# Kernel optimization log

Measured on AMD Instinct MI355X. Metric: run time of the kernel, lower is better.

## Reference

```python
import jax, jax.numpy as jnp
import numpy as np

N = 20000   # genes
E = 200000  # global edges
P = 300     # pathways
EP = 2000   # edges per pathway (global node indices)
D = 3       # in_dim == number of omics (forced by nn.Linear(3,1))


def setup_inputs():
    key = jax.random.key(0)
    ks = jax.random.split(key, 20)
    f = lambda i, shape: jax.random.normal(ks[i], shape, dtype=jnp.float32) * 0.1
    return {
        "x": f(0, (N, D)),
        "edge_index": jax.random.randint(ks[1], (2, E), 0, N),
        "path_edges": jax.random.randint(ks[2], (P, 2, EP), 0, N),
        "W_pool": f(3, (D, D)), "b_pool": f(4, (D,)),
        "W_self": f(5, (D, D)), "W_neigh": f(6, (D, D)), "b_conv": f(7, (D,)),
        "sub_Wl": f(8, (P, D, D)), "sub_bl": f(9, (P, D)), "sub_Wr": f(10, (P, D, D)),
        "pool_Wrel": f(11, (P, D, 1)), "pool_Wroot": f(12, (P, D, 1)), "pool_b": f(13, (P, 1)),
        "gate_W": f(14, (P, D, 1)), "gate_b": f(15, (P, 1)),
        "lin_W": f(16, (D, 1)), "lin_b": f(17, (1,)),
        "mlp_W": f(18, (P, 1)), "mlp_b": f(19, (1,)),
    }


def reference(x, edge_index, path_edges, W_pool, b_pool, W_self, W_neigh, b_conv,
              sub_Wl, sub_bl, sub_Wr, pool_Wrel, pool_Wroot, pool_b,
              gate_W, gate_b, lin_W, lin_b, mlp_W, mlp_b):
    n = x.shape[0]
    # add_self_loops on the global edge_index
    loops = jnp.arange(n)
    src = jnp.concatenate([edge_index[0], loops])
    dst = jnp.concatenate([edge_index[1], loops])

    # global SAGEConv with 'pool' aggregator: max_j relu(W_pool h_j), then self + neigh
    hp = jax.nn.relu(x @ W_pool + b_pool)                       # [N,D]
    agg = jax.ops.segment_max(hp[src], dst, num_segments=n)     # [N,D] (self-loops -> no empty segments)
    h = jnp.tanh(x @ W_self + agg @ W_neigh + b_conv)           # [N,D]

    k = int(np.ceil(0.8 * n))  # SAGPooling ratio=0.8 over all N nodes (full x is passed per pathway)

    def per_path(pe, Wl, bl, Wr, Wrel, Wroot, pb, gW, gb):
        s, d = pe[0], pe[1]
        # SAGEConv (mean aggr) on pathway subgraph edges over full node set
        msum = jax.ops.segment_sum(h[s], d, num_segments=n)
        cnt = jax.ops.segment_sum(jnp.ones(s.shape, h.dtype), d, num_segments=n)
        mean = msum / jnp.maximum(cnt, 1.0)[:, None]
        xc = jax.nn.relu(mean @ Wl + bl + h @ Wr)               # [N,D]
        # SAGPooling score via GraphConv (add aggr): W_rel * sum_j x_j + W_root * x + b
        asum = jax.ops.segment_sum(xc[s], d, num_segments=n)
        score = (asum @ Wrel + xc @ Wroot + pb)[:, 0]           # [N]
        topv, perm = jax.lax.top_k(score, k)
        xk = xc[perm] * jnp.tanh(topv)[:, None]                 # [k,D]
        # GlobalAttention readout: softmax gate over kept nodes
        gate = jax.nn.softmax((xk @ gW + gb)[:, 0])             # [k]
        return jax.nn.relu(gate @ xk)                            # [D]

    readout = jax.vmap(per_path)(path_edges, sub_Wl, sub_bl, sub_Wr,
                                 pool_Wrel, pool_Wroot, pool_b, gate_W, gate_b)  # [P,D]
    r = jax.nn.relu(readout @ lin_W + lin_b).T                  # [1,P]
    # mlp: Dropout (identity in eval) -> ReLU -> Linear(P,1) -> Sigmoid
    return jax.nn.sigmoid(jax.nn.relu(r) @ mlp_W + mlp_b)       # [1,1]
```

## Files before the change

kernel.cpp:

```cpp
#include <hip/hip_runtime.h>
#include <math.h>

#define MAXM 2048
#define BMW  640
#define BS   1024
#define NB   2048

__device__ __forceinline__ unsigned fkey(float f){
  unsigned u = __float_as_uint(f);
  return (u & 0x80000000u) ? ~u : (u | 0x80000000u);
}
__device__ __forceinline__ int lbin(float sc, float lo, float scl){
  int b = (int)((sc - lo) * scl);
  return b < 0 ? 0 : (b > NB-1 ? NB-1 : b);
}
__device__ __forceinline__ float fast_tanh(float x){
  float e = __expf(2.f*x);
  return 1.f - 2.f*__builtin_amdgcn_rcpf(e + 1.f);
}
__device__ __forceinline__ void hp_eval(const float* __restrict__ x, int i,
                                        const float* __restrict__ Wp,
                                        const float* __restrict__ bp, float* o){
  float x0 = x[i*3+0], x1 = x[i*3+1], x2 = x[i*3+2];
  #pragma unroll
  for (int j = 0; j < 3; ++j)
    o[j] = fmaxf(x0*Wp[0*3+j] + x1*Wp[1*3+j] + x2*Wp[2*3+j] + bp[j], 0.f);
}

__global__ void k_edge(const float* __restrict__ x, const int* __restrict__ ei,
                       const float* __restrict__ Wp, const float* __restrict__ bp,
                       float* __restrict__ agg, float* __restrict__ acc,
                       unsigned* __restrict__ counter, int E){
  if (blockIdx.x == 0 && threadIdx.x == 0){ acc[0] = 0.f; counter[0] = 0u; }
  int e = blockIdx.x*blockDim.x + threadIdx.x;
  if (e >= E) return;
  int s = ei[e], d = ei[E+e];
  float o[3]; hp_eval(x, s, Wp, bp, o);
  #pragma unroll
  for (int j = 0; j < 3; ++j)
    if (o[j] > 0.f && o[j] > agg[d*4+j])
      atomicMax((int*)&agg[d*4+j], __float_as_int(o[j]));
}

__global__ void k_h2(const float* __restrict__ x, float* __restrict__ hb,
                     const float* __restrict__ Wp, const float* __restrict__ bp,
                     const float* __restrict__ Ws, const float* __restrict__ Wn,
                     const float* __restrict__ bc, int N){
  int i = blockIdx.x*blockDim.x + threadIdx.x;
  if (i >= N) return;
  float hp[3]; hp_eval(x, i, Wp, bp, hp);
  float x0 = x[i*3+0], x1 = x[i*3+1], x2 = x[i*3+2];
  float a0 = fmaxf(hb[i*4+0], hp[0]);
  float a1 = fmaxf(hb[i*4+1], hp[1]);
  float a2 = fmaxf(hb[i*4+2], hp[2]);
  float o[3];
  #pragma unroll
  for (int j = 0; j < 3; ++j){
    float v = x0*Ws[0*3+j] + x1*Ws[1*3+j] + x2*Ws[2*3+j]
            + a0*Wn[0*3+j] + a1*Wn[1*3+j] + a2*Wn[2*3+j] + bc[j];
    o[j] = tanhf(v);
  }
  float4 hv; hv.x = o[0]; hv.y = o[1]; hv.z = o[2]; hv.w = 0.f;
  *reinterpret_cast<float4*>(&hb[i*4]) = hv;
}

__global__ void __launch_bounds__(BS)
k_mega(const float* __restrict__ h, const int* __restrict__ pe,
       const float* __restrict__ sWl, const float* __restrict__ sbl, const float* __restrict__ sWr,
       const float* __restrict__ pWrel, const float* __restrict__ pWroot, const float* __restrict__ pB,
       const float* __restrict__ gW, const float* __restrict__ gB,
       const float* __restrict__ linW, const float* __restrict__ linb,
       const float* __restrict__ mlpW, const float* __restrict__ mlpb,
       float* __restrict__ spG, float* __restrict__ acc, unsigned* __restrict__ counter,
       unsigned* __restrict__ out, int N, int EP, int K, int P){
  __shared__ unsigned bm[BMW];
  __shared__ int      wpfx[BMW];
  __shared__ float    msum[MAXM*4];
  __shared__ unsigned scrA[NB];
  __shared__ unsigned scrB[NB];
  __shared__ unsigned candIdx[NB];
  __shared__ float    wredf[(BS/64)*2];
  __shared__ float    wredA[(BS/64)*4];
  __shared__ float    wredB[(BS/64)*4];
  __shared__ float    s_mn, s_mx;
  __shared__ float    rlo[3], rsc[3];
  __shared__ int      rb[3];
  __shared__ int      s_r, s_C, s_cc, s_done, s_fused;
  __shared__ unsigned s_uT;

  const int p = blockIdx.x;
  const int tid = threadIdx.x;

  float Wl[9], Wr[9], bl[3], wrel[3], wroot[3], gw[3];
  #pragma unroll
  for (int j = 0; j < 9; ++j){ Wl[j] = sWl[p*9+j]; Wr[j] = sWr[p*9+j]; }
  #pragma unroll
  for (int j = 0; j < 3; ++j){
    bl[j] = sbl[p*3+j]; wrel[j] = pWrel[p*3+j];
    wroot[j] = pWroot[p*3+j]; gw[j] = gW[p*3+j];
  }
  float pbv = pB[p], gbv = gB[p];
  float* sp = spG + (size_t)p*N;

  int*   cnt  = (int*)scrA;
  float* adot = (float*)scrB;

  for (int s = tid; s < MAXM; s += BS){
    cnt[s] = 0; adot[s] = 0.f;
    float4 z; z.x = 0.f; z.y = 0.f; z.z = 0.f; z.w = 0.f;
    *reinterpret_cast<float4*>(&msum[s*4]) = z;
  }
  for (int s = tid; s < BMW; s += BS) bm[s] = 0u;
  if (tid == 0){ s_done = 0; s_fused = 0; s_uT = 0u; }
  __syncthreads();

  const int* ps = pe + (size_t)p*2*EP;
  const int* pd = ps + EP;

  for (int e = tid; e < EP; e += BS) atomicOr(&bm[pd[e]>>5], 1u << (pd[e]&31));
  __syncthreads();
  if (tid < 64){
    int l = tid, base = l*10;
    int c[10], s = 0;
    #pragma unroll
    for (int q = 0; q < 10; ++q){ c[q] = __popc(bm[base+q]); s += c[q]; }
    int pre = s;
    #pragma unroll
    for (int off = 1; off < 64; off <<= 1){
      int t = __shfl_up(pre, off);
      if (l >= off) pre += t;
    }
    pre -= s;
    #pragma unroll
    for (int q = 0; q < 10; ++q){ wpfx[base+q] = pre; pre += c[q]; }
  }
  __syncthreads();
  for (int e = tid; e < EP; e += BS){
    int s = ps[e], d = pd[e];
    int r = wpfx[d>>5] + __popc(bm[d>>5] & ((1u << (d&31)) - 1u));
    float4 hs = *reinterpret_cast<const float4*>(&h[s*4]);
    atomicAdd(&cnt[r], 1);
    atomicAdd(&msum[r*4+0], hs.x);
    atomicAdd(&msum[r*4+1], hs.y);
    atomicAdd(&msum[r*4+2], hs.z);
  }
  __syncthreads();
  for (int r = tid; r < MAXM; r += BS){
    int c = cnt[r];
    cnt[r] = 0;
    if (c > 0){
      float inv = 1.f / (float)c;
      msum[r*4+0] *= inv; msum[r*4+1] *= inv; msum[r*4+2] *= inv;
    }
  }
  __syncthreads();
  for (int e = tid; e < EP; e += BS){
    int s = ps[e], d = pd[e];
    float m0=0.f,m1=0.f,m2=0.f;
    unsigned w = bm[s>>5];
    if ((w >> (s&31)) & 1u){
      int rs = wpfx[s>>5] + __popc(w & ((1u << (s&31)) - 1u));
      float4 mv = *reinterpret_cast<const float4*>(&msum[rs*4]);
      m0 = mv.x; m1 = mv.y; m2 = mv.z;
    }
    float4 hv = *reinterpret_cast<const float4*>(&h[s*4]);
    float h0 = hv.x, h1 = hv.y, h2 = hv.z;
    float x0 = fmaxf(m0*Wl[0]+m1*Wl[3]+m2*Wl[6] + bl[0] + h0*Wr[0]+h1*Wr[3]+h2*Wr[6], 0.f);
    float x1 = fmaxf(m0*Wl[1]+m1*Wl[4]+m2*Wl[7] + bl[1] + h0*Wr[1]+h1*Wr[4]+h2*Wr[7], 0.f);
    float x2 = fmaxf(m0*Wl[2]+m1*Wl[5]+m2*Wl[8] + bl[2] + h0*Wr[2]+h1*Wr[5]+h2*Wr[8], 0.f);
    int rd = wpfx[d>>5] + __popc(bm[d>>5] & ((1u << (d&31)) - 1u));
    atomicAdd(&adot[rd], x0*wrel[0] + x1*wrel[1] + x2*wrel[2]);
  }
  __syncthreads();

  float mn = 3.0e38f, mx = -3.0e38f;
  float tl = 0.f, ta0 = 0.f, ta1 = 0.f, ta2 = 0.f;
  for (int i = tid; i < N; i += BS){
    float m0=0.f,m1=0.f,m2=0.f,ad=0.f;
    unsigned w = bm[i>>5];
    if ((w >> (i&31)) & 1u){
      int r = wpfx[i>>5] + __popc(w & ((1u << (i&31)) - 1u));
      float4 mv = *reinterpret_cast<const float4*>(&msum[r*4]);
      m0 = mv.x; m1 = mv.y; m2 = mv.z;
      ad = adot[r];
    }
    float4 hv = *reinterpret_cast<const float4*>(&h[i*4]);
    float h0 = hv.x, h1 = hv.y, h2 = hv.z;
    float x0 = fmaxf(m0*Wl[0]+m1*Wl[3]+m2*Wl[6] + bl[0] + h0*Wr[0]+h1*Wr[3]+h2*Wr[6], 0.f);
    float x1 = fmaxf(m0*Wl[1]+m1*Wl[4]+m2*Wl[7] + bl[1] + h0*Wr[1]+h1*Wr[4]+h2*Wr[7], 0.f);
    float x2 = fmaxf(m0*Wl[2]+m1*Wl[5]+m2*Wl[8] + bl[2] + h0*Wr[2]+h1*Wr[5]+h2*Wr[8], 0.f);
    float sc = ad + x0*wroot[0]+x1*wroot[1]+x2*wroot[2] + pbv;
    sp[i] = sc;
    mn = fminf(mn, sc); mx = fmaxf(mx, sc);
    float tt = fast_tanh(sc);
    float g = fminf(fmaxf(tt*(x0*gw[0]+x1*gw[1]+x2*gw[2]) + gbv, -60.f), 60.f);
    float e = __expf(g);
    float et = e * tt;
    tl += e; ta0 += et*x0; ta1 += et*x1; ta2 += et*x2;
  }
  #pragma unroll
  for (int off = 32; off > 0; off >>= 1){
    mn  = fminf(mn, __shfl_down(mn, off));
    mx  = fmaxf(mx, __shfl_down(mx, off));
    tl  += __shfl_down(tl,  off); ta0 += __shfl_down(ta0, off);
    ta1 += __shfl_down(ta1, off); ta2 += __shfl_down(ta2, off);
  }
  if ((tid & 63) == 0){
    int w = tid >> 6;
    wredf[w*2+0] = mn; wredf[w*2+1] = mx;
    wredA[w*4+0]=tl; wredA[w*4+1]=ta0; wredA[w*4+2]=ta1; wredA[w*4+3]=ta2;
  }
  __syncthreads();
  if (tid == 0){
    float a = 3.0e38f, b = -3.0e38f;
    for (int w = 0; w < BS/64; ++w){ a = fminf(a, wredf[w*2+0]); b = fmaxf(b, wredf[w*2+1]); }
    s_mn = a; s_mx = b; s_r = K;
    if (!(b > a)){ s_uT = fkey(a); s_done = 1; s_fused = 1; }
  }
  __syncthreads();

  unsigned* hist = scrA;
  unsigned* cand = scrB;

  float dl = 0.f, d0 = 0.f, d1 = 0.f, d2 = 0.f;

  for (int t = 0; t < 3; ++t){
    __syncthreads();
    if (s_done) break;
    float lo, hi;
    if (t == 0){ lo = s_mn; hi = s_mx; }
    else { lo = rlo[t-1] + rb[t-1]/rsc[t-1]; hi = rlo[t-1] + (rb[t-1]+1)/rsc[t-1]; }
    float scl = 2047.0f / (hi - lo);
    if (!(hi > lo) || !(scl < 1e37f)){
      if (tid == 0){ s_uT = fkey(lo); s_done = 1; }
      __syncthreads();
      continue;
    }
    if (t > 0){
      for (int b = tid; b < NB; b += BS) hist[b] = 0u;
      __syncthreads();
    }
    if (t == 0){
      if ((N & 3) == 0){
        int G = N >> 2;
        for (int g = tid; g < G; g += BS){
          float4 v = ((const float4*)sp)[g];
          atomicAdd(&hist[lbin(v.x, lo, scl)], 1u);
          atomicAdd(&hist[lbin(v.y, lo, scl)], 1u);
          atomicAdd(&hist[lbin(v.z, lo, scl)], 1u);
          atomicAdd(&hist[lbin(v.w, lo, scl)], 1u);
        }
      } else {
        for (int i = tid; i < N; i += BS) atomicAdd(&hist[lbin(sp[i], lo, scl)], 1u);
      }
    } else {
      for (int i = tid; i < N; i += BS){
        float sc = sp[i];
        bool act = true;
        for (int q = 0; q < t; ++q) act = act && (lbin(sc, rlo[q], rsc[q]) == rb[q]);
        if (act) atomicAdd(&hist[lbin(sc, lo, scl)], 1u);
      }
    }
    __syncthreads();
    if (tid < 64){
      int l = tid;
      unsigned s = 0;
      for (int q = 0; q < 32; ++q) s += hist[l*32+q];
      unsigned S = s;
      #pragma unroll
      for (int off = 1; off < 64; off <<= 1){
        unsigned u2 = __shfl_down(S, off);
        if (l + off < 64) S += u2;
      }
      unsigned suf = S - s;
      unsigned r = (unsigned)s_r;
      int b = -1; unsigned sufnext = 0, cb = 0;
      for (int q = 31; q >= 0; --q){
        unsigned c = hist[l*32+q];
        unsigned nsuf = suf + c;
        if (nsuf >= r && suf < r){ b = l*32+q; sufnext = suf; cb = c; }
        suf = nsuf;
      }
      if (b >= 0){
        rb[t] = b; rlo[t] = lo; rsc[t] = scl;
        s_r = (int)(r - sufnext);
        s_C = (int)cb;
      }
    }
    __syncthreads();
    int C = s_C;
    if (C <= NB){
      if (tid < 1024) hist[tid] = 0u;
      if (tid == 0) s_cc = 0;
      __syncthreads();
      if (t == 0 && (N & 3) == 0){
        const int b0 = rb[0];
        const float l0 = rlo[0], s0 = rsc[0];
        int G = N >> 2;
        for (int g = tid; g < G; g += BS){
          float4 v = ((const float4*)sp)[g];
          #pragma unroll
          for (int u = 0; u < 4; ++u){
            float sc = (u==0)?v.x:((u==1)?v.y:((u==2)?v.z:v.w));
            int b = lbin(sc, l0, s0);
            if (b == b0){
              int ix = atomicAdd(&s_cc, 1);
              if (ix < NB){ cand[ix] = fkey(sc); candIdx[ix] = (unsigned)(g*4+u); }
            } else if (b < b0){
              int i = g*4+u;
              float m0=0.f,m1=0.f,m2=0.f;
              unsigned w = bm[i>>5];
              if ((w >> (i&31)) & 1u){
                int r = wpfx[i>>5] + __popc(w & ((1u << (i&31)) - 1u));
                float4 mv = *reinterpret_cast<const float4*>(&msum[r*4]);
                m0 = mv.x; m1 = mv.y; m2 = mv.z;
              }
              float4 hv = *reinterpret_cast<const float4*>(&h[i*4]);
              float h0 = hv.x, h1 = hv.y, h2 = hv.z;
              float x0 = fmaxf(m0*Wl[0]+m1*Wl[3]+m2*Wl[6] + bl[0] + h0*Wr[0]+h1*Wr[3]+h2*Wr[6], 0.f);
              float x1 = fmaxf(m0*Wl[1]+m1*Wl[4]+m2*Wl[7] + bl[1] + h0*Wr[1]+h1*Wr[4]+h2*Wr[7], 0.f);
              float x2 = fmaxf(m0*Wl[2]+m1*Wl[5]+m2*Wl[8] + bl[2] + h0*Wr[2]+h1*Wr[5]+h2*Wr[8], 0.f);
              float tt = fast_tanh(sc);
              float gg = fminf(fmaxf(tt*(x0*gw[0]+x1*gw[1]+x2*gw[2]) + gbv, -60.f), 60.f);
              float e = __expf(gg);
              float et = e * tt;
              dl += e; d0 += et*x0; d1 += et*x1; d2 += et*x2;
            }
          }
        }
      } else {
        for (int i = tid; i < N; i += BS){
          float sc = sp[i];
          bool iscand = true, isdrop = false;
          for (int q = 0; q <= t; ++q){
            int b = lbin(sc, rlo[q], rsc[q]);
            if (b != rb[q]){ iscand = false; isdrop = (b < rb[q]); break; }
          }
          if (iscand){
            int ix = atomicAdd(&s_cc, 1);
            if (ix < NB){ cand[ix] = fkey(sc); candIdx[ix] = (unsigned)i; }
          } else if (isdrop){
            float m0=0.f,m1=0.f,m2=0.f;
            unsigned w = bm[i>>5];
            if ((w >> (i&31)) & 1u){
              int r = wpfx[i>>5] + __popc(w & ((1u << (i&31)) - 1u));
              float4 mv = *reinterpret_cast<const float4*>(&msum[r*4]);
              m0 = mv.x; m1 = mv.y; m2 = mv.z;
            }
            float4 hv = *reinterpret_cast<const float4*>(&h[i*4]);
            float h0 = hv.x, h1 = hv.y, h2 = hv.z;
            float x0 = fmaxf(m0*Wl[0]+m1*Wl[3]+m2*Wl[6] + bl[0] + h0*Wr[0]+h1*Wr[3]+h2*Wr[6], 0.f);
            float x1 = fmaxf(m0*Wl[1]+m1*Wl[4]+m2*Wl[7] + bl[1] + h0*Wr[1]+h1*Wr[4]+h2*Wr[7], 0.f);
            float x2 = fmaxf(m0*Wl[2]+m1*Wl[5]+m2*Wl[8] + bl[2] + h0*Wr[2]+h1*Wr[5]+h2*Wr[8], 0.f);
            float tt = fast_tanh(sc);
            float gg = fminf(fmaxf(tt*(x0*gw[0]+x1*gw[1]+x2*gw[2]) + gbv, -60.f), 60.f);
            float e = __expf(gg);
            float et = e * tt;
            dl += e; d0 += et*x0; d1 += et*x1; d2 += et*x2;
          }
        }
      }
      __syncthreads();
      if (tid < 64){
        int l = tid;
        unsigned pref = 0u, mask = 0u;
        int r = s_r;
        #pragma unroll
        for (int pass = 0; pass < 4; ++pass){
          int shift = 24 - 8*pass;
          unsigned* hp = hist + (pass << 8);
          for (int j = l; j < C; j += 64){
            unsigned u = cand[j];
            if ((u & mask) == pref) atomicAdd(&hp[(u>>shift)&255u], 1u);
          }
          asm volatile("s_waitcnt lgkmcnt(0)" ::: "memory");
          unsigned h0 = hp[4*l+0], h1 = hp[4*l+1], h2 = hp[4*l+2], h3 = hp[4*l+3];
          unsigned ssum = h0+h1+h2+h3;
          unsigned S = ssum;
          #pragma unroll
          for (int off = 1; off < 64; off <<= 1){
            unsigned u2 = __shfl_down(S, off);
            if (l + off < 64) S += u2;
          }
          unsigned Snext = S - ssum;
          unsigned rr = (unsigned)r;
          unsigned suf3 = h3 + Snext;
          unsigned suf2 = h2 + suf3;
          unsigned suf1 = h1 + suf2;
          unsigned suf0 = h0 + suf1;
          int b = -1; unsigned sufn = 0;
          if      (suf3 >= rr && Snext < rr){ b = 4*l+3; sufn = Snext; }
          else if (suf2 >= rr && suf3  < rr){ b = 4*l+2; sufn = suf3; }
          else if (suf1 >= rr && suf2  < rr){ b = 4*l+1; sufn = suf2; }
          else if (suf0 >= rr && suf1  < rr){ b = 4*l+0; sufn = suf1; }
          unsigned long long ball = __ballot(b >= 0);
          int src = __ffsll(ball) - 1;
          b    = __shfl(b, src);
          sufn = (unsigned)__shfl((int)sufn, src);
          pref |= (unsigned)b << shift;
          mask |= 255u << shift;
          r = (int)(rr - sufn);
        }
        if (l == 0) s_uT = pref;
      }
      if (tid == 0){ s_done = 1; s_fused = 1; }
      __syncthreads();
      {
        const unsigned uTl = s_uT;
        for (int j = tid; j < C; j += BS){
          if (cand[j] < uTl){
            int i = (int)candIdx[j];
            float sc = sp[i];
            float m0=0.f,m1=0.f,m2=0.f;
            unsigned w = bm[i>>5];
            if ((w >> (i&31)) & 1u){
              int r = wpfx[i>>5] + __popc(w & ((1u << (i&31)) - 1u));
              float4 mv = *reinterpret_cast<const float4*>(&msum[r*4]);
              m0 = mv.x; m1 = mv.y; m2 = mv.z;
            }
            float4 hv = *reinterpret_cast<const float4*>(&h[i*4]);
            float h0 = hv.x, h1 = hv.y, h2 = hv.z;
            float x0 = fmaxf(m0*Wl[0]+m1*Wl[3]+m2*Wl[6] + bl[0] + h0*Wr[0]+h1*Wr[3]+h2*Wr[6], 0.f);
            float x1 = fmaxf(m0*Wl[1]+m1*Wl[4]+m2*Wl[7] + bl[1] + h0*Wr[1]+h1*Wr[4]+h2*Wr[7], 0.f);
            float x2 = fmaxf(m0*Wl[2]+m1*Wl[5]+m2*Wl[8] + bl[2] + h0*Wr[2]+h1*Wr[5]+h2*Wr[8], 0.f);
            float tt = fast_tanh(sc);
            float gg = fminf(fmaxf(tt*(x0*gw[0]+x1*gw[1]+x2*gw[2]) + gbv, -60.f), 60.f);
            float e = __expf(gg);
            float et = e * tt;
            dl += e; d0 += et*x0; d1 += et*x1; d2 += et*x2;
          }
        }
      }
    } else if (t == 2){
      if (tid == 0){ s_uT = fkey(lo + rb[t]/scl); s_done = 1; }
      __syncthreads();
    }
  }
  __syncthreads();
  const unsigned uT = s_uT;

  if (!s_fused){
    for (int i = tid; i < N; i += BS){
      float sc = sp[i];
      if (fkey(sc) < uT){
        float m0=0.f,m1=0.f,m2=0.f;
        unsigned w = bm[i>>5];
        if ((w >> (i&31)) & 1u){
          int r = wpfx[i>>5] + __popc(w & ((1u << (i&31)) - 1u));
          float4 mv = *reinterpret_cast<const float4*>(&msum[r*4]);
          m0 = mv.x; m1 = mv.y; m2 = mv.z;
        }
        float4 hv = *reinterpret_cast<const float4*>(&h[i*4]);
        float h0 = hv.x, h1 = hv.y, h2 = hv.z;
        float x0 = fmaxf(m0*Wl[0]+m1*Wl[3]+m2*Wl[6] + bl[0] + h0*Wr[0]+h1*Wr[3]+h2*Wr[6], 0.f);
        float x1 = fmaxf(m0*Wl[1]+m1*Wl[4]+m2*Wl[7] + bl[1] + h0*Wr[1]+h1*Wr[4]+h2*Wr[7], 0.f);
        float x2 = fmaxf(m0*Wl[2]+m1*Wl[5]+m2*Wl[8] + bl[2] + h0*Wr[2]+h1*Wr[5]+h2*Wr[8], 0.f);
        float tt = fast_tanh(sc);
        float gg = fminf(fmaxf(tt*(x0*gw[0]+x1*gw[1]+x2*gw[2]) + gbv, -60.f), 60.f);
        float e = __expf(gg);
        float et = e * tt;
        dl += e; d0 += et*x0; d1 += et*x1; d2 += et*x2;
      }
    }
  }
  #pragma unroll
  for (int off = 32; off > 0; off >>= 1){
    dl += __shfl_down(dl, off); d0 += __shfl_down(d0, off);
    d1 += __shfl_down(d1, off); d2 += __shfl_down(d2, off);
  }
  if ((tid & 63) == 0){
    int w = tid >> 6;
    wredB[w*4+0]=dl; wredB[w*4+1]=d0; wredB[w*4+2]=d1; wredB[w*4+3]=d2;
  }
  __syncthreads();
  if (tid == 0){
    float L=0.f, A0=0.f, A1=0.f, A2=0.f;
    for (int w = 0; w < BS/64; ++w){
      L  += wredA[w*4+0] - wredB[w*4+0];
      A0 += wredA[w*4+1] - wredB[w*4+1];
      A1 += wredA[w*4+2] - wredB[w*4+2];
      A2 += wredA[w*4+3] - wredB[w*4+3];
    }
    float inv = 1.f / L;
    float r0 = fmaxf(A0*inv, 0.f);
    float r1 = fmaxf(A1*inv, 0.f);
    float r2 = fmaxf(A2*inv, 0.f);
    float rr = fmaxf(r0*linW[0] + r1*linW[1] + r2*linW[2] + linb[0], 0.f);
    atomicAdd(acc, rr * mlpW[p]);
    __threadfence();
    unsigned old = atomicAdd(counter, 1u);
    if (old == (unsigned)(P-1)){
      __threadfence();
      float z = atomicAdd(acc, 0.f) + mlpb[0];
      float a = 1.f / (1.f + expf(-z));
      unsigned A = __float_as_uint(a);
      unsigned B = (A + 0x7FFFu + ((A >> 16) & 1u)) >> 16;
      out[0] = (A & 0xFFFF0000u) | (B & 0xFFFFu);
    }
  }
}

extern "C" void kernel_launch(void* const* d_in, const int* in_sizes, int n_in,
                              void* d_out, int out_size, void* d_ws, size_t ws_size,
                              hipStream_t stream){
  const float* x      = (const float*)d_in[0];
  const int*   ei     = (const int*)  d_in[1];
  const int*   pe     = (const int*)  d_in[2];
  const float* W_pool = (const float*)d_in[3];
  const float* b_pool = (const float*)d_in[4];
  const float* W_self = (const float*)d_in[5];
  const float* W_neigh= (const float*)d_in[6];
  const float* b_conv = (const float*)d_in[7];
  const float* sWl    = (const float*)d_in[8];
  const float* sbl    = (const float*)d_in[9];
  const float* sWr    = (const float*)d_in[10];
  const float* pWrel  = (const float*)d_in[11];
  const float* pWroot = (const float*)d_in[12];
  const float* pB     = (const float*)d_in[13];
  const float* gW     = (const float*)d_in[14];
  const float* gB     = (const float*)d_in[15];
  const float* linW   = (const float*)d_in[16];
  const float* linb   = (const float*)d_in[17];
  const float* mlpW   = (const float*)d_in[18];
  const float* mlpb   = (const float*)d_in[19];

  const int N  = in_sizes[0] / 3;
  const int E  = in_sizes[1] / 2;
  const int P  = in_sizes[13];
  const int EP = in_sizes[2] / (2 * P);
  const int K  = (4*N + 4) / 5;

  float*    ws      = (float*)d_ws;
  float*    acc     = ws;
  unsigned* counter = (unsigned*)(ws + 1);
  float*    agg     = ws + 16;
  float*    h       = agg;
  float*    spG     = ws + 16 + (size_t)4*N;

  k_edge<<<(E+255)/256, 256, 0, stream>>>(x, ei, W_pool, b_pool, agg, acc, counter, E);
  k_h2  <<<(N+255)/256, 256, 0, stream>>>(x, agg, W_pool, b_pool,
                                          W_self, W_neigh, b_conv, N);
  k_mega<<<P, BS, 0, stream>>>(h, pe, sWl, sbl, sWr, pWrel, pWroot, pB, gW, gB,
                               linW, linb, mlpW, mlpb,
                               spG, acc, counter, (unsigned*)d_out, N, EP, K, P);
}
```

Baseline: 234.7 us.

## Fuse first top-k histogram pass into score loop using sampled range

Estimates the score range from a strided sample of one node per thread, then builds the first radix-select histogram inside the main score loop instead of in a separate pass that rereads all scores from global memory. Clamped edge bins are refined on the second pass using the true min and max. This removes one full read of the per-pathway score array. In exchange it adds an extra sample evaluation, a block reduction and two barriers, and the first histogram may have coarser resolution when the sampled range is narrower than the true range.

Result: faster. 229.7 us (median of 2 runs) (-2.1%).

```diff
diff --git a/kernel.cpp b/kernel.cpp
--- a/kernel.cpp
+++ b/kernel.cpp
@@ -83,6 +83,7 @@
   __shared__ float    wredA[(BS/64)*4];
   __shared__ float    wredB[(BS/64)*4];
   __shared__ float    s_mn, s_mx;
+  __shared__ float    s_slo, s_sscl;
   __shared__ float    rlo[3], rsc[3];
   __shared__ int      rb[3];
   __shared__ int      s_r, s_C, s_cc, s_done, s_fused;
@@ -102,8 +103,10 @@
   float pbv = pB[p], gbv = gB[p];
   float* sp = spG + (size_t)p*N;
 
-  int*   cnt  = (int*)scrA;
-  float* adot = (float*)scrB;
+  int*      cnt  = (int*)scrA;
+  float*    adot = (float*)scrB;
+  unsigned* hist = scrA;
+  unsigned* cand = scrB;
 
   for (int s = tid; s < MAXM; s += BS){
     cnt[s] = 0; adot[s] = 0.f;
@@ -173,6 +176,48 @@
   }
   __syncthreads();
 
+  {
+    int i = (int)(((long long)tid * (long long)N) / BS);
+    float m0=0.f,m1=0.f,m2=0.f,ad=0.f;
+    unsigned w = bm[i>>5];
+    if ((w >> (i&31)) & 1u){
+      int r = wpfx[i>>5] + __popc(w & ((1u << (i&31)) - 1u));
+      float4 mv = *reinterpret_cast<const float4*>(&msum[r*4]);
+      m0 = mv.x; m1 = mv.y; m2 = mv.z;
+      ad = adot[r];
+    }
+    float4 hv = *reinterpret_cast<const float4*>(&h[i*4]);
+    float h0 = hv.x, h1 = hv.y, h2 = hv.z;
+    float x0 = fmaxf(m0*Wl[0]+m1*Wl[3]+m2*Wl[6] + bl[0] + h0*Wr[0]+h1*Wr[3]+h2*Wr[6], 0.f);
+    float x1 = fmaxf(m0*Wl[1]+m1*Wl[4]+m2*Wl[7] + bl[1] + h0*Wr[1]+h1*Wr[4]+h2*Wr[7], 0.f);
+    float x2 = fmaxf(m0*Wl[2]+m1*Wl[5]+m2*Wl[8] + bl[2] + h0*Wr[2]+h1*Wr[5]+h2*Wr[8], 0.f);
+    float sc = ad + x0*wroot[0]+x1*wroot[1]+x2*wroot[2] + pbv;
+    float smn = sc, smx = sc;
+    #pragma unroll
+    for (int off = 32; off > 0; off >>= 1){
+      smn = fminf(smn, __shfl_down(smn, off));
+      smx = fmaxf(smx, __shfl_down(smx, off));
+    }
+    if ((tid & 63) == 0){ int w2 = tid >> 6; wredf[w2*2+0] = smn; wredf[w2*2+1] = smx; }
+    __syncthreads();
+    if (tid == 0){
+      float a = 3.0e38f, b = -3.0e38f;
+      for (int w2 = 0; w2 < BS/64; ++w2){
+        a = fminf(a, wredf[w2*2+0]); b = fmaxf(b, wredf[w2*2+1]);
+      }
+      float span = b - a;
+      if (!(span > 0.f)) span = fabsf(a)*1e-6f + 1e-30f;
+      s_slo = a; s_sscl = 2047.0f / span;
+    }
+    __syncthreads();
+  }
+  float lo0, scl0;
+  {
+    unsigned ulo = __builtin_amdgcn_readfirstlane(__float_as_uint(s_slo));
+    unsigned usc = __builtin_amdgcn_readfirstlane(__float_as_uint(s_sscl));
+    lo0 = __uint_as_float(ulo); scl0 = __uint_as_float(usc);
+  }
+
   float mn = 3.0e38f, mx = -3.0e38f;
   float tl = 0.f, ta0 = 0.f, ta1 = 0.f, ta2 = 0.f;
   for (int i = tid; i < N; i += BS){
@@ -191,6 +236,7 @@
     float x2 = fmaxf(m0*Wl[2]+m1*Wl[5]+m2*Wl[8] + bl[2] + h0*Wr[2]+h1*Wr[5]+h2*Wr[8], 0.f);
     float sc = ad + x0*wroot[0]+x1*wroot[1]+x2*wroot[2] + pbv;
     sp[i] = sc;
+    atomicAdd(&hist[lbin(sc, lo0, scl0)], 1u);
     mn = fminf(mn, sc); mx = fmaxf(mx, sc);
     float tt = fast_tanh(sc);
     float g = fminf(fmaxf(tt*(x0*gw[0]+x1*gw[1]+x2*gw[2]) + gbv, -60.f), 60.f);
@@ -219,49 +265,38 @@
   }
   __syncthreads();
 
-  unsigned* hist = scrA;
-  unsigned* cand = scrB;
-
   float dl = 0.f, d0 = 0.f, d1 = 0.f, d2 = 0.f;
 
   for (int t = 0; t < 3; ++t){
     __syncthreads();
     if (s_done) break;
-    float lo, hi;
-    if (t == 0){ lo = s_mn; hi = s_mx; }
-    else { lo = rlo[t-1] + rb[t-1]/rsc[t-1]; hi = rlo[t-1] + (rb[t-1]+1)/rsc[t-1]; }
-    float scl = 2047.0f / (hi - lo);
-    if (!(hi > lo) || !(scl < 1e37f)){
-      if (tid == 0){ s_uT = fkey(lo); s_done = 1; }
-      __syncthreads();
-      continue;
-    }
-    if (t > 0){
+    float lo, scl;
+    if (t == 0){
+      lo = s_slo; scl = s_sscl;
+    } else {
+      float plo = rlo[t-1], pscl = rsc[t-1]; int pb = rb[t-1];
+      lo = plo + pb/pscl;
+      float hi = plo + (pb+1)/pscl;
+      if (t == 1){
+        if (pb == 0)    lo = s_mn;
+        if (pb == NB-1) hi = s_mx;
+      }
+      scl = 2047.0f / (hi - lo);
+      if (!(hi > lo) || !(scl < 1e37f)){
+        if (tid == 0){ s_uT = fkey(lo); s_done = 1; }
+        __syncthreads();
+        continue;
+      }
       for (int b = tid; b < NB; b += BS) hist[b] = 0u;
       __syncthreads();
-    }
-    if (t == 0){
-      if ((N & 3) == 0){
-        int G = N >> 2;
-        for (int g = tid; g < G; g += BS){
-          float4 v = ((const float4*)sp)[g];
-          atomicAdd(&hist[lbin(v.x, lo, scl)], 1u);
-          atomicAdd(&hist[lbin(v.y, lo, scl)], 1u);
-          atomicAdd(&hist[lbin(v.z, lo, scl)], 1u);
-          atomicAdd(&hist[lbin(v.w, lo, scl)], 1u);
-        }
-      } else {
-        for (int i = tid; i < N; i += BS) atomicAdd(&hist[lbin(sp[i], lo, scl)], 1u);
-      }
-    } else {
       for (int i = tid; i < N; i += BS){
         float sc = sp[i];
         bool act = true;
         for (int q = 0; q < t; ++q) act = act && (lbin(sc, rlo[q], rsc[q]) == rb[q]);
         if (act) atomicAdd(&hist[lbin(sc, lo, scl)], 1u);
       }
-    }
-    __syncthreads();
+      __syncthreads();
+    }
     if (tid < 64){
       int l = tid;
       unsigned s = 0;
```
